# Kernel optimization log

Measured on AMD Instinct MI355X. Metric: run time of the kernel, lower is better.

Reference implementation:

```python
import jax, jax.numpy as jnp
import numpy as np

POOL = (7, 7, 3)          # (py, px, pz) pool_size
N_LEVELS = 4              # pyramid_levels = [0,1,2,3]


def setup_inputs() -> dict:
    key = jax.random.key(0)
    ks = jax.random.split(key, 8)
    B, C = 2, 48
    shapes = [(96, 96, 48), (48, 48, 24), (24, 24, 12), (12, 12, 6)]
    fm = {f"fmap{i}": jax.random.normal(ks[i], (B, C) + shapes[i], jnp.float32)
          for i in range(N_LEVELS)}
    N = 1200
    ctr = jax.random.uniform(ks[4], (N, 3), minval=0.15, maxval=0.85)
    sz = jax.random.uniform(ks[5], (N, 3), minval=0.05, maxval=0.5)
    lo = jnp.clip(ctr - sz / 2, 0.0, 1.0)
    hi = jnp.clip(ctr + sz / 2, 0.0, 1.0)
    bix = jax.random.randint(ks[6], (N,), 0, B).astype(jnp.float32)
    # rois: (N, (y1, x1, y2, x2, z1, z2, batch_ix)) normalized coords
    rois = jnp.stack([lo[:, 0], lo[:, 1], hi[:, 0], hi[:, 1],
                      lo[:, 2], hi[:, 2], bix], axis=1)
    return {**fm, "rois": rois}


def _roi_align_3d(fmap, boxes, bix, pool):
    """fmap: (B,C,Y,X,Z); boxes: (N,6) in fmap pixel coords; bix: (N,) int32.
    Trilinear roi_align, sampling one point per bin center. Returns (N,C,py,px,pz)."""
    B, C, Y, X, Z = fmap.shape
    py, px, pz = pool
    N = boxes.shape[0]
    y1, x1, y2, x2, z1, z2 = (boxes[:, i] for i in range(6))

    def centers(a, b, n):
        binsz = (b - a) / n
        return a[:, None] + (jnp.arange(n, dtype=boxes.dtype) + 0.5) * binsz[:, None]

    ys = centers(y1, y2, py)  # (N, py)
    xs = centers(x1, x2, px)  # (N, px)
    zs = centers(z1, z2, pz)  # (N, pz)
    S = py * px * pz
    yy = jnp.broadcast_to(ys[:, :, None, None], (N, py, px, pz)).reshape(N, S)
    xx = jnp.broadcast_to(xs[:, None, :, None], (N, py, px, pz)).reshape(N, S)
    zz = jnp.broadcast_to(zs[:, None, None, :], (N, py, px, pz)).reshape(N, S)

    valid = ((yy > -1.0) & (yy < Y) & (xx > -1.0) & (xx < X)
             & (zz > -1.0) & (zz < Z))
    yc = jnp.clip(yy, 0.0, Y - 1)
    xc = jnp.clip(xx, 0.0, X - 1)
    zc = jnp.clip(zz, 0.0, Z - 1)

    y0 = jnp.floor(yc).astype(jnp.int32); y1i = jnp.minimum(y0 + 1, Y - 1)
    x0 = jnp.floor(xc).astype(jnp.int32); x1i = jnp.minimum(x0 + 1, X - 1)
    z0 = jnp.floor(zc).astype(jnp.int32); z1i = jnp.minimum(z0 + 1, Z - 1)
    ly = yc - y0; hy = 1.0 - ly
    lx = xc - x0; hx = 1.0 - lx
    lz = zc - z0; hz = 1.0 - lz

    fm = jnp.transpose(fmap, (0, 2, 3, 4, 1))  # (B,Y,X,Z,C)
    b = jnp.broadcast_to(bix[:, None], (N, S))

    def g(yi, xi, zi):
        return fm[b, yi, xi, zi]  # (N,S,C)

    val = (g(y0, x0, z0) * (hy * hx * hz)[..., None]
           + g(y0, x0, z1i) * (hy * hx * lz)[..., None]
           + g(y0, x1i, z0) * (hy * lx * hz)[..., None]
           + g(y0, x1i, z1i) * (hy * lx * lz)[..., None]
           + g(y1i, x0, z0) * (ly * hx * hz)[..., None]
           + g(y1i, x0, z1i) * (ly * hx * lz)[..., None]
           + g(y1i, x1i, z0) * (ly * lx * hz)[..., None]
           + g(y1i, x1i, z1i) * (ly * lx * lz)[..., None])
    val = jnp.where(valid[..., None], val, 0.0)
    return jnp.transpose(val.reshape(N, py, px, pz, C), (0, 4, 1, 2, 3))


def reference(fmap0, fmap1, fmap2, fmap3, rois):
    fmaps = [fmap0, fmap1, fmap2, fmap3]
    boxes = rois[:, :6]
    bix = rois[:, 6].astype(jnp.int32)
    h = boxes[:, 2] - boxes[:, 0]
    w = boxes[:, 3] - boxes[:, 1]
    # roi_level = round(4 + log2(sqrt(h*w))).clamp(levels[0], levels[-1])
    roi_level = jnp.clip(jnp.round(4.0 + 0.5 * jnp.log2(h * w)),
                         0, N_LEVELS - 1).astype(jnp.int32)
    out = jnp.zeros((rois.shape[0], fmap0.shape[1]) + POOL, rois.dtype)
    for lvl, fmap in enumerate(fmaps):
        Y, X, Z = fmap.shape[2:]
        scale = jnp.array([Y, X, Y, X, Z, Z], dtype=rois.dtype)
        pooled = _roi_align_3d(fmap, boxes * scale, bix, POOL)
        sel = (roi_level == lvl)[:, None, None, None, None]
        out = out + jnp.where(sel, pooled, 0.0)
    # Equivalent to the torch code's per-level index_select + concat + sort
    # reassembly: output is in original roi order.
    return out
```

## Files before the change

### kernel.cpp

```cpp
#include <hip/hip_runtime.h>

#define PY 7
#define PX 7
#define PZ 3
#define S_BINS 147
#define C_CH   48
#define PER_ROI 7056
#define NCHUNK 4
#define CPT    12
#define TPR    (S_BINS * NCHUNK)

__global__ __launch_bounds__(256) void roialign3d_kernel(
    const float* __restrict__ f0, const float* __restrict__ f1,
    const float* __restrict__ f2, const float* __restrict__ f3,
    const float* __restrict__ rois, float* __restrict__ out, int total)
{
    int t = blockIdx.x * blockDim.x + threadIdx.x;
    if (t >= total) return;

    unsigned n   = (unsigned)t / TPR;
    unsigned rem = (unsigned)t - n * TPR;
    unsigned cs  = rem / S_BINS;
    unsigned s   = rem - cs * S_BINS;

    const float* r = rois + n * 7;
    float by1 = r[0], bx1 = r[1], by2 = r[2], bx2 = r[3], bz1 = r[4], bz2 = r[5];
    int b = (int)r[6];

    float h = by2 - by1, w = bx2 - bx1;
    float lv = rintf(4.0f + 0.5f * log2f(h * w));
    lv = fminf(fmaxf(lv, 0.0f), 3.0f);
    int level = (int)lv;

    const float* fm; int Y, X, Z;
    switch (level) {
        case 0: fm = f0; Y = 96; X = 96; Z = 48; break;
        case 1: fm = f1; Y = 48; X = 48; Z = 24; break;
        case 2: fm = f2; Y = 24; X = 24; Z = 12; break;
        default: fm = f3; Y = 12; X = 12; Z = 6;  break;
    }

    int ybin = s / (PX * PZ);
    int rs   = s - ybin * (PX * PZ);
    int xbin = rs / PZ;
    int zbin = rs - xbin * PZ;

    float fy1 = by1 * Y, fy2 = by2 * Y;
    float fx1 = bx1 * X, fx2 = bx2 * X;
    float fz1 = bz1 * Z, fz2 = bz2 * Z;

    float yy = fy1 + (ybin + 0.5f) * (fy2 - fy1) * (1.0f / PY);
    float xx = fx1 + (xbin + 0.5f) * (fx2 - fx1) * (1.0f / PX);
    float zz = fz1 + (zbin + 0.5f) * (fz2 - fz1) * (1.0f / PZ);

    bool valid = (yy > -1.0f) && (yy < (float)Y) &&
                 (xx > -1.0f) && (xx < (float)X) &&
                 (zz > -1.0f) && (zz < (float)Z);

    float yc = fminf(fmaxf(yy, 0.0f), (float)(Y - 1));
    float xc = fminf(fmaxf(xx, 0.0f), (float)(X - 1));
    float zc = fminf(fmaxf(zz, 0.0f), (float)(Z - 1));

    int y0 = (int)floorf(yc);
    int x0 = (int)floorf(xc);
    int z0 = (int)floorf(zc);
    int y1i = min(y0 + 1, Y - 1);
    int x1i = min(x0 + 1, X - 1);

    float ly = yc - (float)y0, lx = xc - (float)x0, lz = zc - (float)z0;
    float hy = 1.0f - ly,      hx = 1.0f - lx,      hz = 1.0f - lz;

    int  zb    = min(z0, Z - 2);
    bool shift = (zb != z0);
    float wlo  = shift ? 0.0f : hz;
    float whi  = shift ? 1.0f : lz;
    if (!valid) { wlo = 0.0f; whi = 0.0f; }

    float w00 = hy * hx, w01 = hy * lx, w10 = ly * hx, w11 = ly * lx;

    const int plane = Y * X * Z;
    const float* base = fm + ((size_t)b * C_CH + cs * CPT) * (size_t)plane;

    const float* p00 = base + (y0  * X + x0 ) * Z + zb;
    const float* p01 = base + (y0  * X + x1i) * Z + zb;
    const float* p10 = base + (y1i * X + x0 ) * Z + zb;
    const float* p11 = base + (y1i * X + x1i) * Z + zb;

    float* op = out + (size_t)n * PER_ROI + (size_t)cs * CPT * S_BINS + s;

    #pragma unroll 4
    for (int c = 0; c < CPT; ++c) {
        float2 v00 = *(const float2*)p00;
        float2 v01 = *(const float2*)p01;
        float2 v10 = *(const float2*)p10;
        float2 v11 = *(const float2*)p11;

        float lo = w00 * v00.x + w01 * v01.x + w10 * v10.x + w11 * v11.x;
        float hi = w00 * v00.y + w01 * v01.y + w10 * v10.y + w11 * v11.y;
        float val = wlo * lo + whi * hi;

        __builtin_nontemporal_store(val, op);

        p00 += plane; p01 += plane; p10 += plane; p11 += plane;
        op += S_BINS;
    }
}

extern "C" void kernel_launch(void* const* d_in, const int* in_sizes, int n_in,
                              void* d_out, int out_size, void* d_ws, size_t ws_size,
                              hipStream_t stream) {
    const float* f0   = (const float*)d_in[0];
    const float* f1   = (const float*)d_in[1];
    const float* f2   = (const float*)d_in[2];
    const float* f3   = (const float*)d_in[3];
    const float* rois = (const float*)d_in[4];
    float* out = (float*)d_out;

    int n_rois = out_size / PER_ROI;
    int total  = n_rois * TPR;
    int block  = 256;
    int grid   = (total + block - 1) / block;
    roialign3d_kernel<<<grid, block, 0, stream>>>(f0, f1, f2, f3, rois, out, total);
}
```

Before: 37.09 us.

## Stage ROI bounding region into LDS per block before trilinear sampling

Each block now handles one ROI and one 12-channel chunk. It cooperatively loads the ROI's y/x/z bounding region of the feature map into shared memory, using power-of-two padded strides, then computes all 1764 outputs from LDS. This replaces scattered global float2 gathers with a coalesced-ish staging load and cheap LDS reads, and falls back to direct global loads when the region exceeds LDS capacity. In exchange it adds a sync, roughly 63 KB of LDS per block that limits occupancy, and a bounding-box load that may fetch more data than the samples use.

After: 117.4 us. +216.4%, slower.

```diff
diff --git a/kernel.cpp b/kernel.cpp
--- a/kernel.cpp
+++ b/kernel.cpp
@@ -6,22 +6,22 @@
 #define S_BINS 147
 #define C_CH   48
 #define PER_ROI 7056
+#define CPT    12
 #define NCHUNK 4
-#define CPT    12
-#define TPR    (S_BINS * NCHUNK)
+#define OUT_PER_BLK (CPT * S_BINS)
+#define LDS_FLOATS 16128
 
 __global__ __launch_bounds__(256) void roialign3d_kernel(
     const float* __restrict__ f0, const float* __restrict__ f1,
     const float* __restrict__ f2, const float* __restrict__ f3,
-    const float* __restrict__ rois, float* __restrict__ out, int total)
+    const float* __restrict__ rois, float* __restrict__ out)
 {
-    int t = blockIdx.x * blockDim.x + threadIdx.x;
-    if (t >= total) return;
+    __shared__ float lds[LDS_FLOATS];
 
-    unsigned n   = (unsigned)t / TPR;
-    unsigned rem = (unsigned)t - n * TPR;
-    unsigned cs  = rem / S_BINS;
-    unsigned s   = rem - cs * S_BINS;
+    const int bid = blockIdx.x;
+    const int n   = bid >> 2;
+    const int cs  = bid & 3;
+    const int tid = threadIdx.x;
 
     const float* r = rois + n * 7;
     float by1 = r[0], bx1 = r[1], by2 = r[2], bx2 = r[3], bz1 = r[4], bz2 = r[5];
@@ -39,70 +39,118 @@
         case 2: fm = f2; Y = 24; X = 24; Z = 12; break;
         default: fm = f3; Y = 12; X = 12; Z = 6;  break;
     }
-
-    int ybin = s / (PX * PZ);
-    int rs   = s - ybin * (PX * PZ);
-    int xbin = rs / PZ;
-    int zbin = rs - xbin * PZ;
-
-    float fy1 = by1 * Y, fy2 = by2 * Y;
-    float fx1 = bx1 * X, fx2 = bx2 * X;
-    float fz1 = bz1 * Z, fz2 = bz2 * Z;
-
-    float yy = fy1 + (ybin + 0.5f) * (fy2 - fy1) * (1.0f / PY);
-    float xx = fx1 + (xbin + 0.5f) * (fx2 - fx1) * (1.0f / PX);
-    float zz = fz1 + (zbin + 0.5f) * (fz2 - fz1) * (1.0f / PZ);
-
-    bool valid = (yy > -1.0f) && (yy < (float)Y) &&
-                 (xx > -1.0f) && (xx < (float)X) &&
-                 (zz > -1.0f) && (zz < (float)Z);
-
-    float yc = fminf(fmaxf(yy, 0.0f), (float)(Y - 1));
-    float xc = fminf(fmaxf(xx, 0.0f), (float)(X - 1));
-    float zc = fminf(fmaxf(zz, 0.0f), (float)(Z - 1));
-
-    int y0 = (int)floorf(yc);
-    int x0 = (int)floorf(xc);
-    int z0 = (int)floorf(zc);
-    int y1i = min(y0 + 1, Y - 1);
-    int x1i = min(x0 + 1, X - 1);
-
-    float ly = yc - (float)y0, lx = xc - (float)x0, lz = zc - (float)z0;
-    float hy = 1.0f - ly,      hx = 1.0f - lx,      hz = 1.0f - lz;
-
-    int  zb    = min(z0, Z - 2);
-    bool shift = (zb != z0);
-    float wlo  = shift ? 0.0f : hz;
-    float whi  = shift ? 1.0f : lz;
-    if (!valid) { wlo = 0.0f; whi = 0.0f; }
-
-    float w00 = hy * hx, w01 = hy * lx, w10 = ly * hx, w11 = ly * lx;
-
     const int plane = Y * X * Z;
     const float* base = fm + ((size_t)b * C_CH + cs * CPT) * (size_t)plane;
 
-    const float* p00 = base + (y0  * X + x0 ) * Z + zb;
-    const float* p01 = base + (y0  * X + x1i) * Z + zb;
-    const float* p10 = base + (y1i * X + x0 ) * Z + zb;
-    const float* p11 = base + (y1i * X + x1i) * Z + zb;
+    float fy1 = by1 * Y, bwy = (by2 * Y - fy1) * (1.0f / PY);
+    float fx1 = bx1 * X, bwx = (bx2 * X - fx1) * (1.0f / PX);
+    float fz1 = bz1 * Z, bwz = (bz2 * Z - fz1) * (1.0f / PZ);
 
-    float* op = out + (size_t)n * PER_ROI + (size_t)cs * CPT * S_BINS + s;
+    float yc0 = fminf(fmaxf(fy1 + 0.5f * bwy, 0.0f), (float)(Y - 1));
+    float yc6 = fminf(fmaxf(fy1 + 6.5f * bwy, 0.0f), (float)(Y - 1));
+    int ymin = (int)floorf(yc0);
+    int ymax = min((int)floorf(yc6) + 1, Y - 1);
+    int NY = ymax - ymin + 1;
 
-    #pragma unroll 4
-    for (int c = 0; c < CPT; ++c) {
-        float2 v00 = *(const float2*)p00;
-        float2 v01 = *(const float2*)p01;
-        float2 v10 = *(const float2*)p10;
-        float2 v11 = *(const float2*)p11;
+    float xc0 = fminf(fmaxf(fx1 + 0.5f * bwx, 0.0f), (float)(X - 1));
+    float xc6 = fminf(fmaxf(fx1 + 6.5f * bwx, 0.0f), (float)(X - 1));
+    int xmin = (int)floorf(xc0);
+    int xmax = min((int)floorf(xc6) + 1, X - 1);
+    int NX = xmax - xmin + 1;
 
-        float lo = w00 * v00.x + w01 * v01.x + w10 * v10.x + w11 * v11.x;
-        float hi = w00 * v00.y + w01 * v01.y + w10 * v10.y + w11 * v11.y;
-        float val = wlo * lo + whi * hi;
+    float zc0 = fminf(fmaxf(fz1 + 0.5f * bwz, 0.0f), (float)(Z - 1));
+    float zc2 = fminf(fmaxf(fz1 + 2.5f * bwz, 0.0f), (float)(Z - 1));
+    int zmin = min((int)floorf(zc0), Z - 2);
+    int zmax = min((int)floorf(zc2), Z - 2) + 1;
+    int NZ = zmax - zmin + 1;
 
-        __builtin_nontemporal_store(val, op);
+    int shift = 32 - __clz(NZ - 1);
+    int RS    = 1 << shift;
+    int lgXP  = (NX > 1) ? (32 - __clz(NX - 1)) : 0;
+    int XP    = 1 << lgXP;
+    int per_ch = (NY << lgXP) << shift;
+    bool use_lds = (CPT * per_ch) <= LDS_FLOATS;
 
-        p00 += plane; p01 += plane; p10 += plane; p11 += plane;
-        op += S_BINS;
+    if (use_lds) {
+        for (int ch = 0; ch < CPT; ++ch) {
+            const float* chb = base + (size_t)ch * plane;
+            float* ldch = lds + ch * per_ch;
+            for (int j = tid; j < per_ch; j += 256) {
+                int yy = j >> (shift + lgXP);
+                int xx = (j >> shift) & (XP - 1);
+                int dz = j & (RS - 1);
+                if (xx < NX && dz < NZ)
+                    ldch[j] = chb[((ymin + yy) * X + (xmin + xx)) * Z + zmin + dz];
+            }
+        }
+        __syncthreads();
+    }
+
+    float* outp = out + (size_t)n * PER_ROI + (size_t)cs * OUT_PER_BLK;
+    float Yf = (float)Y, Xf = (float)X, Zf = (float)Z;
+
+    for (int oi = tid; oi < OUT_PER_BLK; oi += 256) {
+        unsigned c = (unsigned)oi / 147u;
+        unsigned s = (unsigned)oi - c * 147u;
+        int ybin = s / 21;
+        int t2   = s - ybin * 21;
+        int xbin = t2 / 3;
+        int zbin = t2 - xbin * 3;
+
+        float yy = fy1 + (ybin + 0.5f) * bwy;
+        float xx = fx1 + (xbin + 0.5f) * bwx;
+        float zz = fz1 + (zbin + 0.5f) * bwz;
+
+        bool valid = (yy > -1.0f) && (yy < Yf) &&
+                     (xx > -1.0f) && (xx < Xf) &&
+                     (zz > -1.0f) && (zz < Zf);
+
+        float ycl = fminf(fmaxf(yy, 0.0f), Yf - 1.0f);
+        float xcl = fminf(fmaxf(xx, 0.0f), Xf - 1.0f);
+        float zcl = fminf(fmaxf(zz, 0.0f), Zf - 1.0f);
+
+        int y0 = (int)floorf(ycl);
+        int x0 = (int)floorf(xcl);
+        int z0 = (int)floorf(zcl);
+        int y1i = min(y0 + 1, Y - 1);
+        int x1i = min(x0 + 1, X - 1);
+
+        float ly = ycl - (float)y0, lx = xcl - (float)x0, lz = zcl - (float)z0;
+        float hy = 1.0f - ly,       hx = 1.0f - lx,       hz = 1.0f - lz;
+
+        int  zb    = min(z0, Z - 2);
+        bool sh    = (zb != z0);
+        float wlo  = sh ? 0.0f : hz;
+        float whi  = sh ? 1.0f : lz;
+        if (!valid) { wlo = 0.0f; whi = 0.0f; }
+
+        float w00 = hy * hx, w01 = hy * lx, w10 = ly * hx, w11 = ly * lx;
+
+        float val;
+        if (use_lds) {
+            int ry0 = y0  - ymin, ry1 = y1i - ymin;
+            int rx0 = x0  - xmin, rx1 = x1i - xmin;
+            int rz  = zb  - zmin;
+            int cNY = (int)c * NY;
+            int i00 = ((((cNY + ry0) << lgXP) + rx0) << shift) + rz;
+            int i01 = ((((cNY + ry0) << lgXP) + rx1) << shift) + rz;
+            int i10 = ((((cNY + ry1) << lgXP) + rx0) << shift) + rz;
+            int i11 = ((((cNY + ry1) << lgXP) + rx1) << shift) + rz;
+            float lo = w00 * lds[i00]     + w01 * lds[i01]     + w10 * lds[i10]     + w11 * lds[i11];
+            float hi = w00 * lds[i00 + 1] + w01 * lds[i01 + 1] + w10 * lds[i10 + 1] + w11 * lds[i11 + 1];
+            val = wlo * lo + whi * hi;
+        } else {
+            const float* p = base + (size_t)c * plane;
+            const float2 v00 = *(const float2*)(p + (y0  * X + x0 ) * Z + zb);
+            const float2 v01 = *(const float2*)(p + (y0  * X + x1i) * Z + zb);
+            const float2 v10 = *(const float2*)(p + (y1i * X + x0 ) * Z + zb);
+            const float2 v11 = *(const float2*)(p + (y1i * X + x1i) * Z + zb);
+            float lo = w00 * v00.x + w01 * v01.x + w10 * v10.x + w11 * v11.x;
+            float hi = w00 * v00.y + w01 * v01.y + w10 * v10.y + w11 * v11.y;
+            val = wlo * lo + whi * hi;
+        }
+
+        __builtin_nontemporal_store(val, &outp[oi]);
     }
 }
 
@@ -117,8 +165,6 @@
     float* out = (float*)d_out;
 
     int n_rois = out_size / PER_ROI;
-    int total  = n_rois * TPR;
-    int block  = 256;
-    int grid   = (total + block - 1) / block;
-    roialign3d_kernel<<<grid, block, 0, stream>>>(f0, f1, f2, f3, rois, out, total);
+    int grid   = n_rois * NCHUNK;
+    roialign3d_kernel<<<grid, 256, 0, stream>>>(f0, f1, f2, f3, rois, out);
 }
```

## Split x-corner gathers across thread pairs and combine via lane shuffle

Applied to the files above, without the earlier changes.

Each bin is now handled by a pair of adjacent lanes, each loading one x-corner (two float2 gathers instead of four) over all 48 channels, then summing the partials with __shfl_xor. Only the even lane stores the result. The channel-chunk split is removed, so each thread now loops over all 48 channels instead of 12. This spreads the gathers across more lanes for memory parallelism, at the cost of half the lanes idling on stores, an extra shuffle per channel, and a longer serial loop per thread.

After: 39.61 us. +6.8%, slower.

```diff
diff --git a/kernel.cpp b/kernel.cpp
--- a/kernel.cpp
+++ b/kernel.cpp
@@ -6,9 +6,7 @@
 #define S_BINS 147
 #define C_CH   48
 #define PER_ROI 7056
-#define NCHUNK 4
-#define CPT    12
-#define TPR    (S_BINS * NCHUNK)
+#define TPR    294
 
 __global__ __launch_bounds__(256) void roialign3d_kernel(
     const float* __restrict__ f0, const float* __restrict__ f1,
@@ -20,8 +18,8 @@
 
     unsigned n   = (unsigned)t / TPR;
     unsigned rem = (unsigned)t - n * TPR;
-    unsigned cs  = rem / S_BINS;
-    unsigned s   = rem - cs * S_BINS;
+    unsigned s   = rem >> 1;
+    unsigned cx  = rem & 1;
 
     const float* r = rois + n * 7;
     float by1 = r[0], bx1 = r[1], by2 = r[2], bx2 = r[3], bz1 = r[4], bz2 = r[5];
@@ -76,32 +74,37 @@
     float whi  = shift ? 1.0f : lz;
     if (!valid) { wlo = 0.0f; whi = 0.0f; }
 
-    float w00 = hy * hx, w01 = hy * lx, w10 = ly * hx, w11 = ly * lx;
+    int   xcr = cx ? x1i : x0;
+    float wx  = cx ? lx  : hx;
+    float wA  = hy * wx;
+    float wB  = ly * wx;
 
     const int plane = Y * X * Z;
-    const float* base = fm + ((size_t)b * C_CH + cs * CPT) * (size_t)plane;
+    const float* base = fm + (size_t)b * C_CH * plane;
 
-    const float* p00 = base + (y0  * X + x0 ) * Z + zb;
-    const float* p01 = base + (y0  * X + x1i) * Z + zb;
-    const float* p10 = base + (y1i * X + x0 ) * Z + zb;
-    const float* p11 = base + (y1i * X + x1i) * Z + zb;
+    const float* p0 = base + (y0  * X + xcr) * Z + zb;
+    const float* p1 = base + (y1i * X + xcr) * Z + zb;
 
-    float* op = out + (size_t)n * PER_ROI + (size_t)cs * CPT * S_BINS + s;
+    float* op = out + (size_t)n * PER_ROI + s;
 
-    #pragma unroll 4
-    for (int c = 0; c < CPT; ++c) {
-        float2 v00 = *(const float2*)p00;
-        float2 v01 = *(const float2*)p01;
-        float2 v10 = *(const float2*)p10;
-        float2 v11 = *(const float2*)p11;
+    #pragma unroll 8
+    for (int c = 0; c < C_CH; ++c) {
+        float2 va = *(const float2*)p0;
+        float2 vb = *(const float2*)p1;
 
-        float lo = w00 * v00.x + w01 * v01.x + w10 * v10.x + w11 * v11.x;
-        float hi = w00 * v00.y + w01 * v01.y + w10 * v10.y + w11 * v11.y;
+        float plo = wA * va.x + wB * vb.x;
+        float phi = wA * va.y + wB * vb.y;
+
+        float qlo = __shfl_xor(plo, 1, 64);
+        float qhi = __shfl_xor(phi, 1, 64);
+
+        float lo = plo + qlo;
+        float hi = phi + qhi;
         float val = wlo * lo + whi * hi;
 
-        __builtin_nontemporal_store(val, op);
+        if (cx == 0) __builtin_nontemporal_store(val, op);
 
-        p00 += plane; p01 += plane; p10 += plane; p11 += plane;
+        p0 += plane; p1 += plane;
         op += S_BINS;
     }
 }
```
